# Kernel tuning notes

Measured on AMD Instinct MI355X. Metric: run time of the kernel, lower is better.

## Reference

```python
import jax, jax.numpy as jnp
import numpy as np

B, H, W = 4, 256, 256
TARGET_BETA0 = 5
TARGET_LIFETIME = 0.5
LOSS_SCALE = 100.0


def setup_inputs() -> dict:
    key = jax.random.key(0)
    k1, k2 = jax.random.split(key)
    prob_map = jax.random.uniform(k1, (B, 1, H, W), dtype=jnp.float32)
    roi_mask = (jax.random.uniform(k2, (B, 1, H, W)) < 0.9).astype(jnp.float32)
    return {"prob_map": prob_map, "roi_mask": roi_mask}


def _ph0_topk_loss(f):
    """0-dim persistent homology (V-filtration, 4-connectivity) of f:[H,W],
    then standard top-k MSE(target_lifetime) loss. Equivalent to
    cripser.compute_ph_torch(f, maxdim=0, filtration='V') + _standard_loss.
    Algorithm: Kruskal over grid edges with weight max(f[u],f[v]), elder rule.
    All combinatorics run on stop_gradient values; births/deaths are
    differentiable gathers from f at the paired pixel indices."""
    Hh, Ww = f.shape
    N = Hh * Ww
    fv = f.reshape(-1)
    fvc = jax.lax.stop_gradient(fv)

    idx2d = jnp.arange(N, dtype=jnp.int32).reshape(Hh, Ww)
    r_u = idx2d[:, :-1].reshape(-1)  # right edges
    r_v = r_u + 1
    d_u = idx2d[:-1, :].reshape(-1)  # down edges
    d_v = d_u + Ww
    eu = jnp.concatenate([r_u, d_u])
    ev = jnp.concatenate([r_v, d_v])
    ew = jnp.maximum(fvc[eu], fvc[ev])
    order = jnp.argsort(ew)  # process edges by increasing filtration value
    eu, ev = eu[order], ev[order]

    parent0 = jnp.arange(N, dtype=jnp.int32)

    def step(parent, uv):
        u, v = uv[0], uv[1]

        def find(x):
            return jax.lax.while_loop(lambda y: parent[y] != y, lambda y: parent[y], x)

        ru = find(u)
        rv = find(v)
        merge = ru != rv
        # Invariant: a root is the argmin pixel of its component, so
        # fvc[root] is the component's birth value. Elder rule: the root
        # with smaller birth value survives (ties -> smaller index).
        older_u = (fvc[ru] < fvc[rv]) | ((fvc[ru] == fvc[rv]) & (ru < rv))
        keep = jnp.where(older_u, ru, rv)
        die = jnp.where(older_u, rv, ru)
        b_idx = jnp.where(merge, die, -1)  # birth pixel of the dying comp
        d_pix = jnp.where(fvc[u] >= fvc[v], u, v)  # death = max endpoint
        d_idx = jnp.where(merge, d_pix, -1)
        parent = parent.at[die].set(jnp.where(merge, keep, die))
        parent = parent.at[u].set(jnp.where(merge, keep, ru))  # path compression
        parent = parent.at[v].set(jnp.where(merge, keep, rv))
        return parent, (b_idx, d_idx)

    _, (pb, pd_) = jax.lax.scan(step, parent0, jnp.stack([eu, ev], axis=1))

    valid = pb >= 0
    births = fv[jnp.maximum(pb, 0)]
    deaths = fv[jnp.maximum(pd_, 0)]
    life = jnp.where(valid, deaths - births, 0.0)  # lifetimes >= 0

    # sort descending; invalid slots to the end (keys are stop-gradient)
    key_ = jnp.where(valid, jax.lax.stop_gradient(life), -jnp.inf)
    top = jnp.argsort(-key_)[:TARGET_BETA0]
    topk = life[top]
    vk = valid[top]
    n_use = jnp.sum(vk)  # = min(num_finite, target_beta0)
    sq = jnp.where(vk, (topk - TARGET_LIFETIME) ** 2, 0.0)
    return jnp.sum(sq) / jnp.maximum(n_use, 1).astype(f.dtype)


def reference(prob_map, roi_mask):
    prob = prob_map[:, 0] * roi_mask[:, 0]  # roi masking; (1-roi)*0 is a no-op
    filtration = 1.0 - prob
    losses = jax.vmap(_ph0_topk_loss)(filtration)
    return jnp.mean(losses) * LOSS_SCALE
```

## Files before the change

kernel.cpp:

```cpp
#include <hip/hip_runtime.h>
#include <stdint.h>

#define NPIX 65536
#define NRE  65280
#define NE   130560
#define NIMG 4
#define LTPB 1024
#define ETPB 1024
#define NBLK_L (NIMG*32)
#define TPIX 2048
#define EPAD 4096
#define KMAX 4096
#define HSZ  1024
#define LHSZ 2048
typedef unsigned long long u64;

__device__ __forceinline__ int ufind(unsigned* lbl, int x){
  int r = x, c = (int)lbl[r];
  while (c != r){ r = c; c = (int)lbl[r]; }
  while ((int)lbl[x] != r){ int n = (int)lbl[x]; lbl[x] = (unsigned)r; x = n; }
  return r;
}
__device__ __forceinline__ int ufind16(unsigned short* uf, int x){
  int r = x, c = (int)uf[r];
  while (c != r){ r = c; c = (int)uf[r]; }
  while ((int)uf[x] != r){ int n = (int)uf[x]; uf[x] = (unsigned short)r; x = n; }
  return r;
}

__device__ __forceinline__ void merge5(float* a, const float* b){
  float out[5]; int ia = 0, ib = 0;
  #pragma unroll
  for (int k = 0; k < 5; ++k){
    float av = (ia < 5) ? a[ia] : -2.0f;
    float bv = (ib < 5) ? b[ib] : -2.0f;
    if (av >= bv){ out[k] = av; ++ia; } else { out[k] = bv; ++ib; }
  }
  #pragma unroll
  for (int k = 0; k < 5; ++k) a[k] = out[k];
}

__global__ __launch_bounds__(LTPB)
void ph0_local(const float* __restrict__ prob, const float* __restrict__ roi,
               float* __restrict__ Fg, float* __restrict__ LIFEg,
               unsigned* __restrict__ LBLg, u64* __restrict__ LAg,
               unsigned* __restrict__ C, unsigned* __restrict__ C2,
               unsigned* __restrict__ MAPg, unsigned* __restrict__ KGg)
{
  const int blk = blockIdx.x;
  const int img = blk >> 5;
  const int tile = blk & 31;
  const int tr = tile >> 2, tc = tile & 3;
  const int gr0 = tr*32, gc0 = tc*64;
  const int tid = threadIdx.x;
  const int lane = tid & 63;

  const float* pm = prob + img*NPIX;
  const float* rm = roi  + img*NPIX;
  float* F = Fg + img*NPIX;
  float* LIFE = LIFEg + img*NPIX;
  unsigned* LBL = LBLg + img*NPIX;
  unsigned* MAP = MAPg + img*NPIX;
  unsigned* KG  = KGg  + img*NPIX;
  u64* LA = LAg + (size_t)img*NE;

  __shared__ float          sf[TPIX];
  __shared__ unsigned       slbl[TPIX];
  __shared__ unsigned       sme[TPIX];
  __shared__ unsigned short el[2][EPAD];
  __shared__ unsigned       aux[EPAD];
  __shared__ unsigned       bkw[192];
  __shared__ unsigned short bkp[192];
  __shared__ int s_n[3];

  for (int p = tid; p < TPIX; p += LTPB){
    int gp = ((gr0 + (p>>6))<<8) + gc0 + (p&63);
    float fv = 1.0f - pm[gp]*rm[gp];
    sf[p] = fv; slbl[p] = (unsigned)p;
    F[gp] = fv; LIFE[gp] = 0.0f;
  }
  if (tid < 3) s_n[tid] = 0;
  for (int s = tid; s < 192; s += LTPB){
    unsigned wv = 0xFFFFFFFFu; int p = 0; int gq = -1;
    if (s < 32){ if (tc > 0){ p = s*64;        gq = ((gr0+s)<<8)    + gc0 - 1;  } }
    else if (s < 64){ int k=s-32;  if (tc < 3){ p = k*64+63;  gq = ((gr0+k)<<8)  + gc0 + 64; } }
    else if (s < 128){ int k=s-64; if (tr > 0){ p = k;        gq = ((gr0-1)<<8)  + gc0 + k;  } }
    else { int k=s-128;            if (tr < 7){ p = 31*64+k;  gq = ((gr0+32)<<8) + gc0 + k;  } }
    if (gq >= 0){
      int gp = ((gr0 + (p>>6))<<8) + gc0 + (p&63);
      float fp = 1.0f - pm[gp]*rm[gp];
      float fq = 1.0f - pm[gq]*rm[gq];
      wv = __float_as_uint(fmaxf(fp, fq));
    }
    bkw[s] = wv; bkp[s] = (unsigned short)p;
  }
  __syncthreads();

  int M = EPAD, cur = 0;
  for (int rd = 0; rd < 100000; ++rd){
    int nxt = cur ^ 1;
    for (int i = tid; i < TPIX; i += LTPB) sme[i] = 0xFFFFFFFFu;
    if (tid == 0) s_n[(rd+1)%3] = 0;
    __syncthreads();
    if (tid < 192){
      unsigned wv = bkw[tid];
      if (wv != 0xFFFFFFFFu) atomicMin(&sme[ufind(slbl, (int)bkp[tid])], wv);
    }
    int Mpad = (M + 63) & ~63;
    for (int idx = tid; idx < Mpad; idx += LTPB){
      bool keep = false; int e=0,u=0,v=0,a=0,b=0;
      if (idx < M){
        e = (rd == 0) ? idx : (int)el[cur][idx];
        bool valid;
        if (e < 2048){ u=e; v=e+1; valid = ((e&63)!=63); }
        else { u=e-2048; v=u+64; valid = ((u>>6)!=31); }
        if (valid){
          a = ufind(slbl,u); b = ufind(slbl,v);
          if (a != b){
            unsigned wb = __float_as_uint(fmaxf(sf[u],sf[v]));
            atomicMin(&sme[a],wb); atomicMin(&sme[b],wb);
            keep = true;
          }
        }
      }
      u64 m = __ballot(keep);
      if (m){
        int pos0 = __popcll(m & ((1ULL<<lane)-1));
        int leader = __ffsll((long long)m)-1;
        int base = 0;
        if (lane == leader) base = atomicAdd(&s_n[rd%3], __popcll(m));
        base = __shfl(base, leader);
        if (keep){
          el[nxt][base+pos0] = (unsigned short)e;
          aux[base+pos0] = (unsigned)a | ((unsigned)b<<16);
        }
      }
    }
    __syncthreads();
    int n = s_n[rd%3];
    cur = nxt;
    if (n == M || n == 0){ M = n; break; }
    M = n;
    for (int idx = tid; idx < M; idx += LTPB){
      int e = (int)el[cur][idx];
      unsigned ab = aux[idx];
      int a = (int)(ab & 0xFFFFu), b = (int)(ab >> 16);
      int u, v;
      if (e < 2048){ u = e; v = e + 1; } else { u = e - 2048; v = u + 64; }
      float w = fmaxf(sf[u], sf[v]);
      unsigned wb = __float_as_uint(w);
      float fa = sf[a], fb = sf[b];
      bool bd = (fb < fa) || ((fb == fa) && (b < a));
      int die = bd ? a : b, keep = bd ? b : a;
      if (sme[die] == wb){
        slbl[die] = (unsigned)keep;
        int gd = ((gr0 + (die>>6))<<8) + gc0 + (die&63);
        LIFE[gd] = w - (bd ? fa : fb);
      }
    }
    __syncthreads();
  }

  for (int p = tid; p < TPIX; p += LTPB){
    int r = ufind(slbl, p);
    int gp = ((gr0 + (p>>6))<<8) + gc0 + (p&63);
    LBL[gp] = (unsigned)(((gr0 + (r>>6))<<8) + gc0 + (r&63));
  }
  __syncthreads();
  for (int p = tid; p < TPIX; p += LTPB){
    if ((int)slbl[p] == p){
      unsigned pos = atomicAdd(&C2[img], 1u);
      sme[p] = pos;
      unsigned gp = (unsigned)(((gr0 + (p>>6))<<8) + gc0 + (p&63));
      MAP[gp] = pos;
      KG[pos] = gp;
    }
  }
  __syncthreads();

  unsigned* hk = (unsigned*)&el[cur ^ 1][0];
  unsigned* hw = slbl;
  for (int i = tid; i < LHSZ; i += LTPB){ hk[i] = 0xFFFFFFFFu; hw[i] = 0xFFFFFFFFu; }
  __syncthreads();

  unsigned* ctr = &C[img];
  int Mpad2 = (M + 63) & ~63;
  for (int idx = tid; idx < Mpad2; idx += LTPB){
    bool spill = false;
    u64 rec = 0;
    if (idx < M){
      int e = (int)el[cur][idx];
      unsigned ab = aux[idx];
      int a = (int)(ab & 0xFFFFu), b = (int)(ab >> 16);
      int u, v;
      if (e < 2048){ u = e; v = e + 1; } else { u = e - 2048; v = u + 64; }
      unsigned wb = __float_as_uint(fmaxf(sf[u], sf[v]));
      int lo = a < b ? a : b, hi = a < b ? b : a;
      unsigned key = ((unsigned)lo << 11) | (unsigned)hi;
      unsigned h = ((key * 2654435761u) >> 21) & (LHSZ-1);
      bool ins = false;
      #pragma unroll
      for (int t = 0; t < 8; ++t){
        unsigned old = atomicCAS(&hk[h], 0xFFFFFFFFu, key);
        if (old == 0xFFFFFFFFu || old == key){ atomicMin(&hw[h], wb); ins = true; break; }
        h = (h + 1) & (LHSZ-1);
      }
      if (!ins){
        spill = true;
        rec = ((u64)wb << 32) | ((u64)sme[a] << 16) | sme[b];
      }
    }
    u64 m = __ballot(spill);
    if (m){
      int pos0 = __popcll(m & ((1ULL<<lane)-1));
      int leader = __ffsll((long long)m)-1;
      unsigned base = 0;
      if (lane == leader) base = atomicAdd(ctr, (unsigned)__popcll(m));
      base = (unsigned)__shfl((int)base, leader);
      if (spill) LA[base + pos0] = rec;
    }
  }
  __syncthreads();
  for (int h = tid; h < LHSZ; h += LTPB){
    unsigned key = hk[h];
    bool ok = (key != 0xFFFFFFFFu);
    u64 rec = 0;
    if (ok){
      int a = (int)(key >> 11), b = (int)(key & 0x7FFu);
      rec = ((u64)hw[h] << 32) | ((u64)sme[a] << 16) | sme[b];
    }
    u64 m = __ballot(ok);
    if (m){
      int pos0 = __popcll(m & ((1ULL<<lane)-1));
      int leader = __ffsll((long long)m)-1;
      unsigned base = 0;
      if (lane == leader) base = atomicAdd(ctr, (unsigned)__popcll(m));
      base = (unsigned)__shfl((int)base, leader);
      if (ok) LA[base + pos0] = rec;
    }
  }
}

#define RUN_ROUNDS_GLOBAL(UF, ME, RNK)                                       \
  for (int k = tid; k < K; k += ETPB){                                       \
    unsigned g = kg[k];                                                      \
    UF[k] = (unsigned short)k;                                               \
    RNK[k] = ((u64)__float_as_uint(f[g]) << 32) | g;                         \
  }                                                                          \
  __syncthreads();                                                           \
  for (int rd = 0; rd < 70000 && n > 0; ++rd){                               \
    for (int k = tid; k < K; k += ETPB) ME[k] = 0xFFFFFFFFu;                 \
    if (tid == 0) s_n[0] = 0;                                                \
    __syncthreads();                                                         \
    int Mpad = (n + 63) & ~63;                                               \
    for (int idx = tid; idx < Mpad; idx += ETPB){                            \
      bool keep = false; unsigned wb = 0; int a = 0, b = 0;                  \
      if (idx < n){                                                          \
        u64 rec = src[idx];                                                  \
        wb = (unsigned)(rec >> 32);                                          \
        a = (int)((rec >> 16) & 0xFFFFu);                                    \
        b = (int)(rec & 0xFFFFu);                                            \
        a = ufind16(UF, a); b = ufind16(UF, b);                              \
        if (a != b){ atomicMin(&ME[a], wb); atomicMin(&ME[b], wb); keep = true; } \
      }                                                                      \
      u64 m = __ballot(keep);                                                \
      if (m){                                                                \
        int pos0 = __popcll(m & ((1ULL<<lane)-1));                           \
        int leader = __ffsll((long long)m)-1;                                \
        int base = 0;                                                        \
        if (lane == leader) base = atomicAdd(&s_n[0], __popcll(m));          \
        base = __shfl(base, leader);                                         \
        if (keep) dst[base+pos0] = ((u64)wb<<32)|((u64)(unsigned)a<<16)|(unsigned)b; \
      }                                                                      \
    }                                                                        \
    __syncthreads();                                                         \
    int nn = s_n[0];                                                         \
    for (int idx = tid; idx < nn; idx += ETPB){                              \
      u64 rec = dst[idx];                                                    \
      unsigned wb = (unsigned)(rec >> 32);                                   \
      int a = (int)((rec >> 16) & 0xFFFFu);                                  \
      int b = (int)(rec & 0xFFFFu);                                          \
      bool bd = RNK[b] < RNK[a];                                             \
      int die = bd ? a : b, kp = bd ? b : a;                                 \
      if (ME[die] == wb){                                                    \
        UF[die] = (unsigned short)kp;                                        \
        u64 rk = RNK[die];                                                   \
        life[(unsigned)(rk & 0xFFFFFFFFu)] =                                 \
            __uint_as_float(wb) - __uint_as_float((unsigned)(rk >> 32));     \
      }                                                                      \
    }                                                                        \
    __syncthreads();                                                         \
    u64* t = src; src = dst; dst = t; n = nn;                                \
  }

__global__ __launch_bounds__(ETPB)
void ph0_endgame(const float* __restrict__ Fg, float* __restrict__ LIFEg,
                 unsigned* __restrict__ LBLg, unsigned* __restrict__ MAPg,
                 unsigned* __restrict__ KGg, u64* __restrict__ LAg,
                 u64* __restrict__ LBg, u64* __restrict__ GRg,
                 const unsigned* __restrict__ C, const unsigned* __restrict__ C2,
                 float* __restrict__ LOSS, unsigned* __restrict__ DONE,
                 float* __restrict__ out)
{
  const int img = blockIdx.x, tid = threadIdx.x;
  const int lane = tid & 63;
  const float* f = Fg + img*NPIX;
  float* life = LIFEg + img*NPIX;
  unsigned* lblg = LBLg + img*NPIX;
  unsigned* map  = MAPg + img*NPIX;
  const unsigned* kg = KGg + img*NPIX;
  u64* src = LAg + (size_t)img*NE;
  u64* dst = LBg + (size_t)img*NE;
  u64* rnk = GRg + (size_t)img*NPIX;

  __shared__ u64 smem8[7208];
  unsigned short* s_uf = (unsigned short*)smem8;
  unsigned* s_meB = (unsigned*)((char*)smem8 + 8192);
  unsigned* s_hkB = (unsigned*)((char*)smem8 + 40960);
  unsigned* s_hwB = (unsigned*)((char*)smem8 + 49152);
  float*    s_w5  = (float*)((char*)smem8 + 57344);
  __shared__ int s_n[3];

  const int K = (int)C2[img];
  const int nInt = (int)C[img];

  for (int s = tid; s < 2560; s += ETPB){
    int gu, gv;
    if (s < 768){ int ci = s >> 8, row = s & 255, col = 63 + (ci<<6); gu = (row<<8)+col; gv = gu+1; }
    else { int k = s - 768; int ri = k >> 8, colh = k & 255, gr = 31 + (ri<<5); gu = (gr<<8)+colh; gv = gu+256; }
    unsigned ia = map[lblg[gu]];
    unsigned ib = map[lblg[gv]];
    unsigned wb = __float_as_uint(fmaxf(f[gu], f[gv]));
    src[nInt + s] = ((u64)wb << 32) | ((u64)ia << 16) | ib;
  }
  if (tid < 3) s_n[tid] = 0;
  int n = nInt + 2560;

  if (K <= KMAX){
    for (int k = tid; k < K; k += ETPB){
      unsigned g = kg[k];
      s_uf[k] = (unsigned short)k;
      rnk[k] = ((u64)__float_as_uint(f[g]) << 32) | g;
      s_meB[k] = 0xFFFFFFFFu;
    }
    for (int h = tid; h < HSZ; h += ETPB){ s_hkB[h] = 0xFFFFFFFFu; s_hwB[h] = 0xFFFFFFFFu; }
    __syncthreads();

    for (int rd = 0; rd < 70000; ++rd){
      const int bi = rd & 1;
      unsigned* me = s_meB + bi*KMAX;
      unsigned* hk = s_hkB + bi*HSZ;
      unsigned* hw = s_hwB + bi*HSZ;
      const bool useHash = (n > 1024);
      int Mpad = (n + 63) & ~63;
      for (int idx = tid; idx < Mpad; idx += ETPB){
        bool app = false; unsigned wb = 0; int a = 0, b = 0;
        if (idx < n){
          u64 rec = src[idx];
          a = (int)((rec >> 16) & 0xFFFFu);
          b = (int)(rec & 0xFFFFu);
          a = ufind16(s_uf, a); b = ufind16(s_uf, b);
          if (a != b){
            wb = (unsigned)(rec >> 32);
            if (useHash){
              int lo = a < b ? a : b, hi = a < b ? b : a;
              unsigned key = ((unsigned)lo << 12) | (unsigned)hi;
              unsigned h = ((key * 2654435761u) >> 20) & (HSZ-1);
              bool ins = false;
              #pragma unroll
              for (int t = 0; t < 8; ++t){
                unsigned old = atomicCAS(&hk[h], 0xFFFFFFFFu, key);
                if (old == 0xFFFFFFFFu || old == key){ atomicMin(&hw[h], wb); ins = true; break; }
                h = (h + 1) & (HSZ-1);
              }
              if (!ins){ atomicMin(&me[a], wb); atomicMin(&me[b], wb); app = true; }
            } else {
              atomicMin(&me[a], wb); atomicMin(&me[b], wb); app = true;
            }
          }
        }
        u64 m = __ballot(app);
        if (m){
          int pos0 = __popcll(m & ((1ULL<<lane)-1));
          int leader = __ffsll((long long)m)-1;
          int base = 0;
          if (lane == leader) base = atomicAdd(&s_n[rd%3], __popcll(m));
          base = __shfl(base, leader);
          if (app) dst[base+pos0] = ((u64)wb<<32)|((u64)(unsigned)a<<16)|(unsigned)b;
        }
      }
      __syncthreads();
      if (useHash){
        for (int h = tid; h < HSZ; h += ETPB){
          unsigned key = hk[h];
          bool okk = (key != 0xFFFFFFFFu);
          unsigned wb = 0; int a = 0, b = 0;
          if (okk){
            a = (int)(key >> 12); b = (int)(key & 0xFFFu);
            wb = hw[h];
            atomicMin(&me[a], wb); atomicMin(&me[b], wb);
          }
          u64 m = __ballot(okk);
          if (m){
            int pos0 = __popcll(m & ((1ULL<<lane)-1));
            int leader = __ffsll((long long)m)-1;
            int base = 0;
            if (lane == leader) base = atomicAdd(&s_n[rd%3], __popcll(m));
            base = __shfl(base, leader);
            if (okk) dst[base+pos0] = ((u64)wb<<32)|((u64)(unsigned)a<<16)|(unsigned)b;
          }
        }
        __syncthreads();
      }
      int nn = s_n[rd%3];
      if (nn == 0) break;
      for (int idx = tid; idx < nn; idx += ETPB){
        u64 rec = dst[idx];
        unsigned wb = (unsigned)(rec >> 32);
        int a = (int)((rec >> 16) & 0xFFFFu);
        int b = (int)(rec & 0xFFFFu);
        u64 ra = rnk[a], rb = rnk[b];
        bool bd = rb < ra;
        int die = bd ? a : b, kp = bd ? b : a;
        if (me[die] == wb){
          s_uf[die] = (unsigned short)kp;
          u64 rk = bd ? ra : rb;
          life[(unsigned)(rk & 0xFFFFFFFFu)] =
              __uint_as_float(wb) - __uint_as_float((unsigned)(rk >> 32));
        }
      }
      {
        unsigned* meN = s_meB + (bi^1)*KMAX;
        for (int k = tid; k < K; k += ETPB) meN[k] = 0xFFFFFFFFu;
        if (nn > 1024){
          unsigned* hkN = s_hkB + (bi^1)*HSZ;
          unsigned* hwN = s_hwB + (bi^1)*HSZ;
          for (int h = tid; h < HSZ; h += ETPB){ hkN[h] = 0xFFFFFFFFu; hwN[h] = 0xFFFFFFFFu; }
        }
        if (tid == 0) s_n[(rd+1)%3] = 0;
      }
      __syncthreads();
      u64* t = src; src = dst; dst = t;
      n = nn;
    }
  } else {
    __syncthreads();
    unsigned short* g_uf = (unsigned short*)lblg;
    unsigned*       g_me = map;
    u64*            g_rnk = rnk;
    RUN_ROUNDS_GLOBAL(g_uf, g_me, g_rnk)
  }

  float t5[5] = {-1.f,-1.f,-1.f,-1.f,-1.f};
  for (int i = tid; i < NPIX; i += ETPB){
    float v = life[i];
    if (v > t5[4]){
      int j = 4;
      while (j > 0 && t5[j-1] < v){ t5[j] = t5[j-1]; --j; }
      t5[j] = v;
    }
  }
  #pragma unroll
  for (int off = 1; off < 64; off <<= 1){
    float o[5];
    #pragma unroll
    for (int k = 0; k < 5; ++k) o[k] = __shfl_xor(t5[k], off);
    merge5(t5, o);
  }
  if (lane == 0){
    int wv = tid >> 6;
    #pragma unroll
    for (int k = 0; k < 5; ++k) s_w5[wv*5+k] = t5[k];
  }
  __syncthreads();
  if (tid < 64){
    float u5[5];
    #pragma unroll
    for (int k = 0; k < 5; ++k) u5[k] = (tid < ETPB/64) ? s_w5[tid*5+k] : -2.0f;
    #pragma unroll
    for (int off = 1; off < 16; off <<= 1){
      float o[5];
      #pragma unroll
      for (int k = 0; k < 5; ++k) o[k] = __shfl_xor(u5[k], off);
      merge5(u5, o);
    }
    if (tid == 0){
      float lsum = 0.0f;
      #pragma unroll
      for (int k = 0; k < 5; ++k){ float d = u5[k] - 0.5f; lsum += d*d; }
      atomicExch(&LOSS[img], lsum * 0.2f);
      __threadfence();
      unsigned prev = atomicAdd(DONE, 1u);
      if (prev == NIMG - 1){
        float s = 0.0f;
        #pragma unroll
        for (int i = 0; i < NIMG; ++i) s += atomicAdd(&LOSS[i], 0.0f);
        out[0] = s * 25.0f;
      }
    }
  }
}

extern "C" void kernel_launch(void* const* d_in, const int* in_sizes, int n_in,
                              void* d_out, int out_size, void* d_ws, size_t ws_size,
                              hipStream_t stream)
{
  const float* prob = (const float*)d_in[0];
  const float* roi  = (const float*)d_in[1];
  char* ws = (char*)d_ws;
  const size_t SZL = (size_t)4*NE*8;
  float*    F    = (float*)(ws);
  float*    LIFE = (float*)(ws + (1u<<20));
  unsigned* LBL  = (unsigned*)(ws + (2u<<20));
  unsigned* MAP  = (unsigned*)(ws + (3u<<20));
  unsigned* KG   = (unsigned*)(ws + (4u<<20));
  u64*      LA   = (u64*)(ws + (5u<<20));
  u64*      LB   = (u64*)(ws + (5u<<20) + SZL);
  u64*      GR   = (u64*)(ws + (5u<<20) + 2*SZL);
  unsigned* C    = (unsigned*)(ws + (5u<<20) + 2*SZL + (2u<<20));
  unsigned* C2   = C + 4;
  unsigned* DONE = C + 8;
  float*    LOSS = (float*)((char*)C + 64);
  float*    out  = (float*)d_out;

  hipMemsetAsync(C, 0, 64, stream);
  ph0_local<<<NBLK_L, LTPB, 0, stream>>>(prob, roi, F, LIFE, LBL, LA, C, C2, MAP, KG);
  ph0_endgame<<<NIMG, ETPB, 0, stream>>>(F, LIFE, LBL, MAP, KG, LA, LB, GR, C, C2, LOSS, DONE, out);
}
```

Measured before the change: 314.9 us.

## Track top-5 lifetimes on the fly and keep endgame edge lists in LDS

```diff
diff --git a/kernel.cpp b/kernel.cpp
--- a/kernel.cpp
+++ b/kernel.cpp
@@ -13,6 +13,7 @@
 #define KMAX 4096
 #define HSZ  1024
 #define LHSZ 2048
+#define ECAP 4096
 typedef unsigned long long u64;
 
 __device__ __forceinline__ int ufind(unsigned* lbl, int x){
@@ -40,12 +41,21 @@
   for (int k = 0; k < 5; ++k) a[k] = out[k];
 }
 
+__device__ __forceinline__ void ins5(float* t5, float v){
+  if (v > t5[4]){
+    int j = 4;
+    while (j > 0 && t5[j-1] < v){ t5[j] = t5[j-1]; --j; }
+    t5[j] = v;
+  }
+}
+
 __global__ __launch_bounds__(LTPB)
 void ph0_local(const float* __restrict__ prob, const float* __restrict__ roi,
                float* __restrict__ Fg, float* __restrict__ LIFEg,
                unsigned* __restrict__ LBLg, u64* __restrict__ LAg,
                unsigned* __restrict__ C, unsigned* __restrict__ C2,
-               unsigned* __restrict__ MAPg, unsigned* __restrict__ KGg)
+               unsigned* __restrict__ MAPg, unsigned* __restrict__ KGg,
+               float* __restrict__ T5g)
 {
   const int blk = blockIdx.x;
   const int img = blk >> 5;
@@ -66,20 +76,26 @@
 
   __shared__ float          sf[TPIX];
   __shared__ unsigned       slbl[TPIX];
-  __shared__ unsigned       sme[TPIX];
+  __shared__ unsigned       smeb[2][TPIX];
   __shared__ unsigned short el[2][EPAD];
   __shared__ unsigned       aux[EPAD];
   __shared__ unsigned       bkw[192];
   __shared__ unsigned short bkp[192];
+  __shared__ unsigned       s_fired[TPIX/32];
+  __shared__ float          s_t5w[(LTPB/64)*5];
   __shared__ int s_n[3];
+
+  float t5[5] = {-1.f,-1.f,-1.f,-1.f,-1.f};
 
   for (int p = tid; p < TPIX; p += LTPB){
     int gp = ((gr0 + (p>>6))<<8) + gc0 + (p&63);
     float fv = 1.0f - pm[gp]*rm[gp];
     sf[p] = fv; slbl[p] = (unsigned)p;
+    smeb[0][p] = 0xFFFFFFFFu; smeb[1][p] = 0xFFFFFFFFu;
     F[gp] = fv; LIFE[gp] = 0.0f;
   }
   if (tid < 3) s_n[tid] = 0;
+  if (tid < TPIX/32) s_fired[tid] = 0;
   for (int s = tid; s < 192; s += LTPB){
     unsigned wv = 0xFFFFFFFFu; int p = 0; int gq = -1;
     if (s < 32){ if (tc > 0){ p = s*64;        gq = ((gr0+s)<<8)    + gc0 - 1;  } }
@@ -99,9 +115,7 @@
   int M = EPAD, cur = 0;
   for (int rd = 0; rd < 100000; ++rd){
     int nxt = cur ^ 1;
-    for (int i = tid; i < TPIX; i += LTPB) sme[i] = 0xFFFFFFFFu;
-    if (tid == 0) s_n[(rd+1)%3] = 0;
-    __syncthreads();
+    unsigned* sme = smeb[rd & 1];
     if (tid < 192){
       unsigned wv = bkw[tid];
       if (wv != 0xFFFFFFFFu) atomicMin(&sme[ufind(slbl, (int)bkp[tid])], wv);
@@ -155,12 +169,21 @@
       if (sme[die] == wb){
         slbl[die] = (unsigned)keep;
         int gd = ((gr0 + (die>>6))<<8) + gc0 + (die&63);
-        LIFE[gd] = w - (bd ? fa : fb);
-      }
+        float lt = w - (bd ? fa : fb);
+        LIFE[gd] = lt;
+        unsigned bbit = 1u << (die & 31);
+        if (!(atomicOr(&s_fired[die >> 5], bbit) & bbit)) ins5(t5, lt);
+      }
+    }
+    {
+      unsigned* smeN = smeb[(rd+1) & 1];
+      for (int i = tid; i < TPIX; i += LTPB) smeN[i] = 0xFFFFFFFFu;
+      if (tid == 0) s_n[(rd+1)%3] = 0;
     }
     __syncthreads();
   }
 
+  unsigned* posm = smeb[0];
   for (int p = tid; p < TPIX; p += LTPB){
     int r = ufind(slbl, p);
     int gp = ((gr0 + (p>>6))<<8) + gc0 + (p&63);
@@ -170,7 +193,7 @@
   for (int p = tid; p < TPIX; p += LTPB){
     if ((int)slbl[p] == p){
       unsigned pos = atomicAdd(&C2[img], 1u);
-      sme[p] = pos;
+      posm[p] = pos;
       unsigned gp = (unsigned)(((gr0 + (p>>6))<<8) + gc0 + (p&63));
       MAP[gp] = pos;
       KG[pos] = gp;
@@ -207,7 +230,7 @@
       }
       if (!ins){
         spill = true;
-        rec = ((u64)wb << 32) | ((u64)sme[a] << 16) | sme[b];
+        rec = ((u64)wb << 32) | ((u64)posm[a] << 16) | posm[b];
       }
     }
     u64 m = __ballot(spill);
@@ -227,7 +250,7 @@
     u64 rec = 0;
     if (ok){
       int a = (int)(key >> 11), b = (int)(key & 0x7FFu);
-      rec = ((u64)hw[h] << 32) | ((u64)sme[a] << 16) | sme[b];
+      rec = ((u64)hw[h] << 32) | ((u64)posm[a] << 16) | posm[b];
     }
     u64 m = __ballot(ok);
     if (m){
@@ -237,6 +260,36 @@
       if (lane == leader) base = atomicAdd(ctr, (unsigned)__popcll(m));
       base = (unsigned)__shfl((int)base, leader);
       if (ok) LA[base + pos0] = rec;
+    }
+  }
+
+  #pragma unroll
+  for (int off = 1; off < 64; off <<= 1){
+    float o[5];
+    #pragma unroll
+    for (int k = 0; k < 5; ++k) o[k] = __shfl_xor(t5[k], off);
+    merge5(t5, o);
+  }
+  if (lane == 0){
+    int wv = tid >> 6;
+    #pragma unroll
+    for (int k = 0; k < 5; ++k) s_t5w[wv*5+k] = t5[k];
+  }
+  __syncthreads();
+  if (tid < 64){
+    float u5[5];
+    #pragma unroll
+    for (int k = 0; k < 5; ++k) u5[k] = (tid < LTPB/64) ? s_t5w[tid*5+k] : -2.0f;
+    #pragma unroll
+    for (int off = 1; off < 16; off <<= 1){
+      float o[5];
+      #pragma unroll
+      for (int k = 0; k < 5; ++k) o[k] = __shfl_xor(u5[k], off);
+      merge5(u5, o);
+    }
+    if (tid == 0){
+      #pragma unroll
+      for (int k = 0; k < 5; ++k) T5g[blk*5+k] = u5[k];
     }
   }
 }
@@ -299,6 +352,7 @@
                  unsigned* __restrict__ KGg, u64* __restrict__ LAg,
                  u64* __restrict__ LBg, u64* __restrict__ GRg,
                  const unsigned* __restrict__ C, const unsigned* __restrict__ C2,
+                 const float* __restrict__ T5g,
                  float* __restrict__ LOSS, unsigned* __restrict__ DONE,
                  float* __restrict__ out)
 {
@@ -313,12 +367,15 @@
   u64* dst = LBg + (size_t)img*NE;
   u64* rnk = GRg + (size_t)img*NPIX;
 
-  __shared__ u64 smem8[7208];
-  unsigned short* s_uf = (unsigned short*)smem8;
-  unsigned* s_meB = (unsigned*)((char*)smem8 + 8192);
-  unsigned* s_hkB = (unsigned*)((char*)smem8 + 40960);
-  unsigned* s_hwB = (unsigned*)((char*)smem8 + 49152);
-  float*    s_w5  = (float*)((char*)smem8 + 57344);
+  __shared__ unsigned short s_uf[KMAX];
+  __shared__ unsigned s_meB[2*KMAX];
+  __shared__ unsigned s_hkB[2*HSZ];
+  __shared__ unsigned s_hwB[2*HSZ];
+  __shared__ u64 s_rnk[KMAX];
+  __shared__ u64 s_lstA[ECAP];
+  __shared__ u64 s_lstB[ECAP];
+  __shared__ unsigned s_fired[KMAX/32];
+  __shared__ float s_w5[(ETPB/64)*5];
   __shared__ int s_n[3];
 
   const int K = (int)C2[img];
@@ -336,15 +393,22 @@
   if (tid < 3) s_n[tid] = 0;
   int n = nInt + 2560;
 
+  float t5[5] = {-1.f,-1.f,-1.f,-1.f,-1.f};
+
   if (K <= KMAX){
     for (int k = tid; k < K; k += ETPB){
       unsigned g = kg[k];
       s_uf[k] = (unsigned short)k;
-      rnk[k] = ((u64)__float_as_uint(f[g]) << 32) | g;
+      s_rnk[k] = ((u64)__float_as_uint(f[g]) << 32) | g;
       s_meB[k] = 0xFFFFFFFFu;
     }
     for (int h = tid; h < HSZ; h += ETPB){ s_hkB[h] = 0xFFFFFFFFu; s_hwB[h] = 0xFFFFFFFFu; }
+    if (tid < KMAX/32) s_fired[tid] = 0;
+    if (tid < 32*5) ins5(t5, T5g[img*(32*5) + tid]);
     __syncthreads();
+
+    u64 *lsrc = s_lstA, *ldst = s_lstB;
+    bool sL = false;
 
     for (int rd = 0; rd < 70000; ++rd){
       const int bi = rd & 1;
@@ -352,11 +416,12 @@
       unsigned* hk = s_hkB + bi*HSZ;
       unsigned* hw = s_hwB + bi*HSZ;
       const bool useHash = (n > 1024);
+      const bool dL = (n <= ECAP);
       int Mpad = (n + 63) & ~63;
       for (int idx = tid; idx < Mpad; idx += ETPB){
         bool app = false; unsigned wb = 0; int a = 0, b = 0;
         if (idx < n){
-          u64 rec = src[idx];
+          u64 rec = sL ? lsrc[idx] : src[idx];
           a = (int)((rec >> 16) & 0xFFFFu);
           b = (int)(rec & 0xFFFFu);
           a = ufind16(s_uf, a); b = ufind16(s_uf, b);
@@ -386,7 +451,10 @@
           int base = 0;
           if (lane == leader) base = atomicAdd(&s_n[rd%3], __popcll(m));
           base = __shfl(base, leader);
-          if (app) dst[base+pos0] = ((u64)wb<<32)|((u64)(unsigned)a<<16)|(unsigned)b;
+          if (app){
+            u64 r = ((u64)wb<<32)|((u64)(unsigned)a<<16)|(unsigned)b;
+            if (dL) ldst[base+pos0] = r; else dst[base+pos0] = r;
+          }
         }
       }
       __syncthreads();
@@ -407,7 +475,10 @@
             int base = 0;
             if (lane == leader) base = atomicAdd(&s_n[rd%3], __popcll(m));
             base = __shfl(base, leader);
-            if (okk) dst[base+pos0] = ((u64)wb<<32)|((u64)(unsigned)a<<16)|(unsigned)b;
+            if (okk){
+              u64 r = ((u64)wb<<32)|((u64)(unsigned)a<<16)|(unsigned)b;
+              if (dL) ldst[base+pos0] = r; else dst[base+pos0] = r;
+            }
           }
         }
         __syncthreads();
@@ -415,18 +486,20 @@
       int nn = s_n[rd%3];
       if (nn == 0) break;
       for (int idx = tid; idx < nn; idx += ETPB){
-        u64 rec = dst[idx];
+        u64 rec = dL ? ldst[idx] : dst[idx];
         unsigned wb = (unsigned)(rec >> 32);
         int a = (int)((rec >> 16) & 0xFFFFu);
         int b = (int)(rec & 0xFFFFu);
-        u64 ra = rnk[a], rb = rnk[b];
+        u64 ra = s_rnk[a], rb = s_rnk[b];
         bool bd = rb < ra;
         int die = bd ? a : b, kp = bd ? b : a;
         if (me[die] == wb){
           s_uf[die] = (unsigned short)kp;
-          u64 rk = bd ? ra : rb;
-          life[(unsigned)(rk & 0xFFFFFFFFu)] =
-              __uint_as_float(wb) - __uint_as_float((unsigned)(rk >> 32));
+          unsigned bbit = 1u << (die & 31);
+          if (!(atomicOr(&s_fired[die >> 5], bbit) & bbit)){
+            u64 rk = bd ? ra : rb;
+            ins5(t5, __uint_as_float(wb) - __uint_as_float((unsigned)(rk >> 32)));
+          }
         }
       }
       {
@@ -440,7 +513,9 @@
         if (tid == 0) s_n[(rd+1)%3] = 0;
       }
       __syncthreads();
-      u64* t = src; src = dst; dst = t;
+      { u64* t = src; src = dst; dst = t; }
+      { u64* t = lsrc; lsrc = ldst; ldst = t; }
+      sL = dL;
       n = nn;
     }
   } else {
@@ -449,17 +524,9 @@
     unsigned*       g_me = map;
     u64*            g_rnk = rnk;
     RUN_ROUNDS_GLOBAL(g_uf, g_me, g_rnk)
-  }
-
-  float t5[5] = {-1.f,-1.f,-1.f,-1.f,-1.f};
-  for (int i = tid; i < NPIX; i += ETPB){
-    float v = life[i];
-    if (v > t5[4]){
-      int j = 4;
-      while (j > 0 && t5[j-1] < v){ t5[j] = t5[j-1]; --j; }
-      t5[j] = v;
-    }
-  }
+    for (int i = tid; i < NPIX; i += ETPB) ins5(t5, life[i]);
+  }
+
   #pragma unroll
   for (int off = 1; off < 64; off <<= 1){
     float o[5];
@@ -521,9 +588,10 @@
   unsigned* C2   = C + 4;
   unsigned* DONE = C + 8;
   float*    LOSS = (float*)((char*)C + 64);
+  float*    T5   = (float*)(ws + (5u<<20) + 2*SZL - 2560);
   float*    out  = (float*)d_out;
 
   hipMemsetAsync(C, 0, 64, stream);
-  ph0_local<<<NBLK_L, LTPB, 0, stream>>>(prob, roi, F, LIFE, LBL, LA, C, C2, MAP, KG);
-  ph0_endgame<<<NIMG, ETPB, 0, stream>>>(F, LIFE, LBL, MAP, KG, LA, LB, GR, C, C2, LOSS, DONE, out);
-}
+  ph0_local<<<NBLK_L, LTPB, 0, stream>>>(prob, roi, F, LIFE, LBL, LA, C, C2, MAP, KG, T5);
+  ph0_endgame<<<NIMG, ETPB, 0, stream>>>(F, LIFE, LBL, MAP, KG, LA, LB, GR, C, C2, T5, LOSS, DONE, out);
+}
```

Result: faster. 268.8 us (-14.6%).
